# Performance work log

Measured on AMD Instinct MI355X. Metric: run time of the kernel, lower is better.

## Reference

```python
import jax, jax.numpy as jnp
import numpy as np

BN_EPS = 1e-5
NORM_EPS = 1e-6


def _nearest_resize(m, H, W):
    # torch F.interpolate(mode='nearest'): idx = floor(i * in/out)
    B, C, h, w = m.shape
    iy = (jnp.arange(H) * h) // H
    ix = (jnp.arange(W) * w) // W
    return m[:, :, iy][:, :, :, ix]


def _distance_transform(m_s):
    # Euclidean distance of every pixel to nearest foreground pixel (mask>0.5),
    # normalized per-sample to [0,1]; all-background samples -> ones map.
    B, _, H, W = m_s.shape
    HW = H * W
    yy, xx = jnp.meshgrid(jnp.arange(H, dtype=jnp.float32),
                          jnp.arange(W, dtype=jnp.float32), indexing='ij')
    ys, xs = yy.reshape(-1), xx.reshape(-1)
    # shared [HW, HW] pairwise squared distances (same for all batch elems)
    D2 = (ys[:, None] - ys[None, :]) ** 2 + (xs[:, None] - xs[None, :]) ** 2
    fg = m_s.reshape(B, HW) > 0.5                                  # [B, HW]
    min_d2 = jnp.min(jnp.where(fg[:, None, :], D2[None], jnp.inf), axis=-1)  # [B, HW]
    has_fg = fg.any(axis=1, keepdims=True)
    dist = jnp.where(has_fg, jnp.sqrt(min_d2), 1.0)
    mx = dist.max(axis=1, keepdims=True)
    dist = dist / (mx + NORM_EPS)
    return dist.reshape(B, 1, H, W)


def _forward(f_s, supp_feat_bin, support_mask, w_fusion, gamma, beta):
    B, C, H, W = f_s.shape
    m_s = _nearest_resize(support_mask, H, W)
    attn = jax.nn.sigmoid(jnp.sum(f_s * supp_feat_bin, axis=1, keepdims=True))  # [B,1,H,W]
    f_w = f_s * attn
    dist = _distance_transform(m_s)
    fusion_in = jnp.concatenate([f_s, supp_feat_bin, f_w, dist], axis=1)  # [B,3C+1,H,W]
    y = jnp.einsum('oc,bchw->bohw', w_fusion, fusion_in)  # 1x1 conv, no bias
    # BatchNorm2d in training mode: biased batch stats over (B,H,W)
    mean = y.mean(axis=(0, 2, 3))
    var = y.var(axis=(0, 2, 3))
    yn = (y - mean[None, :, None, None]) * jax.lax.rsqrt(var[None, :, None, None] + BN_EPS)
    return jax.nn.relu(yn * gamma[None, :, None, None] + beta[None, :, None, None])


def setup_inputs() -> dict:
    key = jax.random.key(0)
    k1, k2, k3, k4 = jax.random.split(key, 4)
    B, C, H, W = 8, 256, 64, 64
    Hm, Wm = 256, 256
    return {
        'f_s': jax.random.normal(k1, (B, C, H, W), dtype=jnp.float32),
        'supp_feat_bin': jax.random.normal(k2, (B, C, H, W), dtype=jnp.float32),
        'support_mask': jax.random.uniform(k3, (B, 1, Hm, Wm), dtype=jnp.float32),
        'w_fusion': jax.random.normal(k4, (C, 3 * C + 1), dtype=jnp.float32) * 0.02,
        'gamma': jnp.ones((C,), dtype=jnp.float32),
        'beta': jnp.zeros((C,), dtype=jnp.float32),
    }


def reference(f_s, supp_feat_bin, support_mask, w_fusion, gamma, beta):
    return _forward(f_s, supp_feat_bin, support_mask, w_fusion, gamma, beta)
```

## Files before the change

### kernel.cpp

```cpp
#include <hip/hip_runtime.h>
#include <math.h>

#define C_IN   256
#define HW_    4096
#define KW_    769
#define NPIX_BN 32768.0f

typedef short bf16x8 __attribute__((ext_vector_type(8)));
typedef float f32x4  __attribute__((ext_vector_type(4)));
typedef unsigned short u16x4 __attribute__((ext_vector_type(4)));

__device__ inline unsigned short f2bf(float x){
    unsigned u = __float_as_uint(x);
    u += 0x7fffu + ((u >> 16) & 1u);
    return (unsigned short)(u >> 16);
}

__global__ __launch_bounds__(256) void prep_w(
    const float* __restrict__ w, unsigned short* __restrict__ wp)
{
    int idx = blockIdx.x * 256 + threadIdx.x;
    int j  = idx & 7;
    int o  = (idx >> 3) & 255;
    int t2 = idx >> 11;
    int kg = t2 & 3, ks = (t2 >> 2) & 7, m = t2 >> 5;
    int c  = m * 256 + ks * 32 + kg * 8 + j;
    wp[idx] = f2bf(w[(size_t)o * KW_ + c]);
}

__global__ __launch_bounds__(1024) void dist_kernel(
    const float* __restrict__ mask, float* __restrict__ dist_raw,
    unsigned* __restrict__ dmax)
{
    __shared__ float2 fg[4096];
    __shared__ int cnt;
    __shared__ float wmax[16];
    int b = blockIdx.x, tile = blockIdx.y;
    int t = threadIdx.x, lane = t & 63;
    if (t == 0) cnt = 0;
    __syncthreads();
    const float* mb = mask + (size_t)b * 65536;
    #pragma unroll
    for (int r = 0; r < 4; ++r) {
        int pp = r * 1024 + t;
        int i = pp >> 6, j = pp & 63;
        bool pred = mb[i * 1024 + j * 4] > 0.5f;
        unsigned long long bal = __ballot(pred);
        int base = 0;
        if (lane == 0) base = atomicAdd(&cnt, __popcll(bal));
        base = __shfl(base, 0, 64);
        if (pred)
            fg[base + __popcll(bal & ((1ull << lane) - 1ull))] =
                make_float2((float)i, (float)j);
    }
    __syncthreads();
    int nfg = cnt;
    int pix = tile * 256 + (t >> 2);
    int q = t & 3;
    float py = (float)(pix >> 6), px = (float)(pix & 63);
    float m = 3.4e38f;
    for (int it = q; it < nfg; it += 4) {
        float dy = py - fg[it].x;
        float dx = px - fg[it].y;
        m = fminf(m, dy * dy + dx * dx);
    }
    m = fminf(m, __shfl_xor(m, 1, 64));
    m = fminf(m, __shfl_xor(m, 2, 64));
    float d = (nfg == 0) ? 1.0f : sqrtf(m);
    if (q == 0) dist_raw[b * HW_ + pix] = d;
    float mm = d;
    #pragma unroll
    for (int off = 1; off < 64; off <<= 1)
        mm = fmaxf(mm, __shfl_xor(mm, off, 64));
    if (lane == 0) wmax[t >> 6] = mm;
    __syncthreads();
    if (t == 0) {
        float M = wmax[0];
        #pragma unroll
        for (int i = 1; i < 16; ++i) M = fmaxf(M, wmax[i]);
        atomicMax(dmax + b, __float_as_uint(M));
    }
}

__global__ __launch_bounds__(256, 2) void gemm_kernel(
    const float* __restrict__ f_s, const float* __restrict__ sfb,
    const float* __restrict__ w, const unsigned short* __restrict__ wprep,
    const float* __restrict__ dist_raw, const unsigned* __restrict__ dmax,
    float* __restrict__ y, float* __restrict__ gsum, float* __restrict__ gsumsq)
{
    __shared__ unsigned short Lf[2048], Ls[2048];
    __shared__ float attn_sm[4][64];
    __shared__ float attn_fin[64];
    __shared__ float red[2][64][2];

    int bx = blockIdx.x;
    int ot = bx & 1, nt = bx >> 1;
    int oBase = ot * 128;
    int nBase = nt * 64;
    int b = nBase >> 12, pBase = nBase & 4095;
    int t = threadIdx.x;
    int lane = t & 63, g = t >> 6;
    int wo = g >> 1, wn = g & 1;
    int l15 = lane & 15, kq = lane >> 4;

    const float* fB = f_s + (size_t)b * C_IN * HW_ + pBase;
    const float* sB = sfb + (size_t)b * C_IN * HW_ + pBase;

    f32x4 acc[3][4][2];
    #pragma unroll
    for (int m = 0; m < 3; ++m)
        #pragma unroll
        for (int fo = 0; fo < 4; ++fo)
            #pragma unroll
            for (int fn = 0; fn < 2; ++fn)
                acc[m][fo][fn] = (f32x4){0.f, 0.f, 0.f, 0.f};

    float ap = 0.f;
    const bf16x8* WP = (const bf16x8*)wprep;
    const bf16x8* BFr = (const bf16x8*)Lf;
    const bf16x8* BSr = (const bf16x8*)Ls;

    for (int ks = 0; ks < 8; ++ks) {
        {
            const float* fr = fB + (size_t)(ks * 32 + g * 8) * HW_ + lane;
            const float* sr = sB + (size_t)(ks * 32 + g * 8) * HW_ + lane;
            float fv[8], sv[8];
            #pragma unroll
            for (int j = 0; j < 8; ++j) {
                fv[j] = fr[(size_t)j * HW_];
                sv[j] = sr[(size_t)j * HW_];
                ap += fv[j] * sv[j];
            }
            #pragma unroll
            for (int q = 0; q < 2; ++q) {
                u16x4 pf, ps;
                #pragma unroll
                for (int jj = 0; jj < 4; ++jj) {
                    pf[jj] = f2bf(fv[q * 4 + jj]);
                    ps[jj] = f2bf(sv[q * 4 + jj]);
                }
                ((u16x4*)Lf)[(g * 64 + lane) * 2 + q] = pf;
                ((u16x4*)Ls)[(g * 64 + lane) * 2 + q] = ps;
            }
        }
        __syncthreads();
        bf16x8 bf0 = BFr[kq * 64 + wn * 32 + l15];
        bf16x8 bf1 = BFr[kq * 64 + wn * 32 + 16 + l15];
        bf16x8 bs0 = BSr[kq * 64 + wn * 32 + l15];
        bf16x8 bs1 = BSr[kq * 64 + wn * 32 + 16 + l15];
        #pragma unroll
        for (int fo = 0; fo < 4; ++fo) {
            int o = oBase + wo * 64 + fo * 16 + l15;
            bf16x8 a1 = WP[((0 * 8 + ks) * 4 + kq) * 256 + o];
            bf16x8 a2 = WP[((1 * 8 + ks) * 4 + kq) * 256 + o];
            bf16x8 a3 = WP[((2 * 8 + ks) * 4 + kq) * 256 + o];
            acc[0][fo][0] = __builtin_amdgcn_mfma_f32_16x16x32_bf16(a1, bf0, acc[0][fo][0], 0, 0, 0);
            acc[0][fo][1] = __builtin_amdgcn_mfma_f32_16x16x32_bf16(a1, bf1, acc[0][fo][1], 0, 0, 0);
            acc[1][fo][0] = __builtin_amdgcn_mfma_f32_16x16x32_bf16(a2, bs0, acc[1][fo][0], 0, 0, 0);
            acc[1][fo][1] = __builtin_amdgcn_mfma_f32_16x16x32_bf16(a2, bs1, acc[1][fo][1], 0, 0, 0);
            acc[2][fo][0] = __builtin_amdgcn_mfma_f32_16x16x32_bf16(a3, bf0, acc[2][fo][0], 0, 0, 0);
            acc[2][fo][1] = __builtin_amdgcn_mfma_f32_16x16x32_bf16(a3, bf1, acc[2][fo][1], 0, 0, 0);
        }
        __syncthreads();
    }

    attn_sm[g][lane] = ap;
    __syncthreads();
    if (t < 64) {
        float a = attn_sm[0][t] + attn_sm[1][t] + attn_sm[2][t] + attn_sm[3][t];
        attn_fin[t] = 1.f / (1.f + expf(-a));
    }
    __syncthreads();

    float dinv = 1.0f / (__uint_as_float(dmax[b]) + 1e-6f);
    const float* dR = dist_raw + b * HW_ + pBase;
    float at[2], dn[2];
    #pragma unroll
    for (int fn = 0; fn < 2; ++fn) {
        int nb = wn * 32 + fn * 16 + l15;
        at[fn] = attn_fin[nb];
        dn[fn] = dR[nb] * dinv;
    }
    float s_acc[4][4], ss_acc[4][4];
    #pragma unroll
    for (int fo = 0; fo < 4; ++fo) {
        #pragma unroll
        for (int r = 0; r < 4; ++r) {
            int o = oBase + wo * 64 + fo * 16 + kq * 4 + r;
            float wd = w[(size_t)o * KW_ + 768];
            float s = 0.f, ss = 0.f;
            #pragma unroll
            for (int fn = 0; fn < 2; ++fn) {
                float v = acc[0][fo][fn][r] + acc[1][fo][fn][r]
                        + at[fn] * acc[2][fo][fn][r] + wd * dn[fn];
                int nb = wn * 32 + fn * 16 + l15;
                y[((size_t)b * C_IN + o) * HW_ + pBase + nb] = v;
                s += v; ss += v * v;
            }
            s_acc[fo][r] = s; ss_acc[fo][r] = ss;
        }
    }
    #pragma unroll
    for (int m = 8; m; m >>= 1) {
        #pragma unroll
        for (int fo = 0; fo < 4; ++fo)
            #pragma unroll
            for (int r = 0; r < 4; ++r) {
                s_acc[fo][r]  += __shfl_xor(s_acc[fo][r],  m, 64);
                ss_acc[fo][r] += __shfl_xor(ss_acc[fo][r], m, 64);
            }
    }
    if (wn == 1 && l15 == 0) {
        #pragma unroll
        for (int fo = 0; fo < 4; ++fo)
            #pragma unroll
            for (int r = 0; r < 4; ++r) {
                int ol = fo * 16 + kq * 4 + r;
                red[wo][ol][0] = s_acc[fo][r];
                red[wo][ol][1] = ss_acc[fo][r];
            }
    }
    __syncthreads();
    if (wn == 0 && l15 == 0) {
        #pragma unroll
        for (int fo = 0; fo < 4; ++fo)
            #pragma unroll
            for (int r = 0; r < 4; ++r) {
                int ol = fo * 16 + kq * 4 + r;
                int o = oBase + wo * 64 + ol;
                atomicAdd(&gsum[o],   s_acc[fo][r]  + red[wo][ol][0]);
                atomicAdd(&gsumsq[o], ss_acc[fo][r] + red[wo][ol][1]);
            }
    }
}

__global__ __launch_bounds__(256) void bn_kernel(
    const float* __restrict__ gsum, const float* __restrict__ gsumsq,
    const float* __restrict__ gamma, const float* __restrict__ beta,
    float* __restrict__ y)
{
    int bo = blockIdx.x;
    int o = bo & 255;
    float mean = gsum[o] * (1.0f / NPIX_BN);
    float var  = gsumsq[o] * (1.0f / NPIX_BN) - mean * mean;
    float sc = gamma[o] * rsqrtf(var + 1e-5f);
    float sh = beta[o] - mean * sc;
    float4* p = (float4*)(y + (size_t)bo * HW_);
    int t = threadIdx.x;
    #pragma unroll
    for (int r = 0; r < 4; ++r) {
        float4 v = p[r * 256 + t];
        v.x = fmaxf(v.x * sc + sh, 0.f);
        v.y = fmaxf(v.y * sc + sh, 0.f);
        v.z = fmaxf(v.z * sc + sh, 0.f);
        v.w = fmaxf(v.w * sc + sh, 0.f);
        p[r * 256 + t] = v;
    }
}

extern "C" void kernel_launch(void* const* d_in, const int* in_sizes, int n_in,
                              void* d_out, int out_size, void* d_ws, size_t ws_size,
                              hipStream_t stream)
{
    const float* f_s   = (const float*)d_in[0];
    const float* sfb   = (const float*)d_in[1];
    const float* mask  = (const float*)d_in[2];
    const float* w     = (const float*)d_in[3];
    const float* gamma = (const float*)d_in[4];
    const float* beta  = (const float*)d_in[5];
    float* out = (float*)d_out;
    float* ws  = (float*)d_ws;

    float*          dist_raw = ws;
    unsigned*       dmax     = (unsigned*)(ws + 32768);
    float*          gsum     = ws + 32784;
    float*          gsumsq   = ws + 33040;
    unsigned short* wprep    = (unsigned short*)(ws + 33296);

    hipMemsetAsync(ws + 32768, 0, (33296 - 32768) * 4, stream);

    prep_w<<<768, 256, 0, stream>>>(w, wprep);
    dist_kernel<<<dim3(8, 16), 1024, 0, stream>>>(mask, dist_raw, dmax);
    gemm_kernel<<<1024, 256, 0, stream>>>(f_s, sfb, w, wprep, dist_raw, dmax,
                                          out, gsum, gsumsq);
    bn_kernel<<<2048, 256, 0, stream>>>(gsum, gsumsq, gamma, beta, out);
}
```

Baseline: 247.0 us.

## Double-buffer LDS tiles and prefetch next K-slice into registers in fused GEMM

The GEMM main loop now keeps two LDS buffers for the bf16 f_s/sfb tiles and loads the next K-slice's global values into registers while the current slice's MFMAs run. This drops one barrier per iteration and is meant to hide global load latency behind matrix work. It also switches the sigmoid to the fast __expf intrinsic and renames a variable in the weight prep. In exchange it uses more LDS and holds more live registers, which could lower occupancy under the 2-waves launch bound.

```diff
diff --git a/kernel.cpp b/kernel.cpp
--- a/kernel.cpp
+++ b/kernel.cpp
@@ -23,8 +23,8 @@
     int j  = idx & 7;
     int o  = (idx >> 3) & 255;
     int t2 = idx >> 11;
-    int kg = t2 & 3, ks = (t2 >> 2) & 7, m = t2 >> 5;
-    int c  = m * 256 + ks * 32 + kg * 8 + j;
+    int kq = t2 & 3, ks = (t2 >> 2) & 7, m = t2 >> 5;
+    int c  = m * 256 + ks * 32 + kq * 8 + j;
     wp[idx] = f2bf(w[(size_t)o * KW_ + c]);
 }
 
@@ -88,7 +88,7 @@
     const float* __restrict__ dist_raw, const unsigned* __restrict__ dmax,
     float* __restrict__ y, float* __restrict__ gsum, float* __restrict__ gsumsq)
 {
-    __shared__ unsigned short Lf[2048], Ls[2048];
+    __shared__ unsigned short Lf[2][2048], Ls[2][2048];
     __shared__ float attn_sm[4][64];
     __shared__ float attn_fin[64];
     __shared__ float red[2][64][2];
@@ -103,8 +103,8 @@
     int wo = g >> 1, wn = g & 1;
     int l15 = lane & 15, kq = lane >> 4;
 
-    const float* fB = f_s + (size_t)b * C_IN * HW_ + pBase;
-    const float* sB = sfb + (size_t)b * C_IN * HW_ + pBase;
+    const float* fB = f_s + (size_t)b * C_IN * HW_ + pBase + lane;
+    const float* sB = sfb + (size_t)b * C_IN * HW_ + pBase + lane;
 
     f32x4 acc[3][4][2];
     #pragma unroll
@@ -117,33 +117,40 @@
 
     float ap = 0.f;
     const bf16x8* WP = (const bf16x8*)wprep;
-    const bf16x8* BFr = (const bf16x8*)Lf;
-    const bf16x8* BSr = (const bf16x8*)Ls;
-
+
+    float fv[8], sv[8];
+    #pragma unroll
+    for (int j = 0; j < 8; ++j) {
+        fv[j] = fB[(size_t)(g * 8 + j) * HW_];
+        sv[j] = sB[(size_t)(g * 8 + j) * HW_];
+    }
+
+    #pragma unroll
     for (int ks = 0; ks < 8; ++ks) {
-        {
-            const float* fr = fB + (size_t)(ks * 32 + g * 8) * HW_ + lane;
-            const float* sr = sB + (size_t)(ks * 32 + g * 8) * HW_ + lane;
-            float fv[8], sv[8];
+        int cur = ks & 1;
+        #pragma unroll
+        for (int j = 0; j < 8; ++j) ap += fv[j] * sv[j];
+        #pragma unroll
+        for (int q = 0; q < 2; ++q) {
+            u16x4 pf, ps;
+            #pragma unroll
+            for (int jj = 0; jj < 4; ++jj) {
+                pf[jj] = f2bf(fv[q * 4 + jj]);
+                ps[jj] = f2bf(sv[q * 4 + jj]);
+            }
+            ((u16x4*)Lf[cur])[(g * 64 + lane) * 2 + q] = pf;
+            ((u16x4*)Ls[cur])[(g * 64 + lane) * 2 + q] = ps;
+        }
+        __syncthreads();
+        if (ks < 7) {
             #pragma unroll
             for (int j = 0; j < 8; ++j) {
-                fv[j] = fr[(size_t)j * HW_];
-                sv[j] = sr[(size_t)j * HW_];
-                ap += fv[j] * sv[j];
-            }
-            #pragma unroll
-            for (int q = 0; q < 2; ++q) {
-                u16x4 pf, ps;
-                #pragma unroll
-                for (int jj = 0; jj < 4; ++jj) {
-                    pf[jj] = f2bf(fv[q * 4 + jj]);
-                    ps[jj] = f2bf(sv[q * 4 + jj]);
-                }
-                ((u16x4*)Lf)[(g * 64 + lane) * 2 + q] = pf;
-                ((u16x4*)Ls)[(g * 64 + lane) * 2 + q] = ps;
-            }
-        }
-        __syncthreads();
+                fv[j] = fB[(size_t)((ks + 1) * 32 + g * 8 + j) * HW_];
+                sv[j] = sB[(size_t)((ks + 1) * 32 + g * 8 + j) * HW_];
+            }
+        }
+        const bf16x8* BFr = (const bf16x8*)Lf[cur];
+        const bf16x8* BSr = (const bf16x8*)Ls[cur];
         bf16x8 bf0 = BFr[kq * 64 + wn * 32 + l15];
         bf16x8 bf1 = BFr[kq * 64 + wn * 32 + 16 + l15];
         bf16x8 bs0 = BSr[kq * 64 + wn * 32 + l15];
@@ -161,14 +168,14 @@
             acc[2][fo][0] = __builtin_amdgcn_mfma_f32_16x16x32_bf16(a3, bf0, acc[2][fo][0], 0, 0, 0);
             acc[2][fo][1] = __builtin_amdgcn_mfma_f32_16x16x32_bf16(a3, bf1, acc[2][fo][1], 0, 0, 0);
         }
-        __syncthreads();
-    }
-
+    }
+
+    __syncthreads();
     attn_sm[g][lane] = ap;
     __syncthreads();
     if (t < 64) {
         float a = attn_sm[0][t] + attn_sm[1][t] + attn_sm[2][t] + attn_sm[3][t];
-        attn_fin[t] = 1.f / (1.f + expf(-a));
+        attn_fin[t] = 1.f / (1.f + __expf(-a));
     }
     __syncthreads();
 
```

Result: no change. 245.5 us (-0.6%).
